# Optimization experiments

Measured on AMD Instinct MI355X. Metric: run time of the kernel, lower is better.

## Reference

```python
import jax, jax.numpy as jnp
import numpy as np
from jax import lax

B, T, I, H, O = 256, 512, 64, 128, 2  # batch, seq_len, input_size, hidden_size, output_size


def gru_layer(x, Wih, Whh, bih, bhh, reverse):
    # x: [B,T,in_dim], Wih: [3H,in_dim], Whh: [3H,H]; PyTorch gate order: r, z, n
    xw = jnp.einsum('bti,gi->btg', x, Wih) + bih  # precompute input projections [B,T,3H]

    def step(h, xw_t):
        gh = h @ Whh.T + bhh  # [B,3H]
        r = jax.nn.sigmoid(xw_t[:, :H] + gh[:, :H])
        z = jax.nn.sigmoid(xw_t[:, H:2 * H] + gh[:, H:2 * H])
        n = jnp.tanh(xw_t[:, 2 * H:] + r * gh[:, 2 * H:])
        h_new = (1.0 - z) * n + z * h
        return h_new, h_new

    h0 = jnp.zeros((x.shape[0], H), x.dtype)
    _, hs = lax.scan(step, h0, jnp.swapaxes(xw, 0, 1), reverse=reverse)
    # lax.scan with reverse=True stacks outputs aligned to original time order,
    # matching PyTorch's bidirectional GRU output layout.
    return jnp.swapaxes(hs, 0, 1)  # [B,T,H]


def gru_forward(x, params, fc_w, fc_b):
    h = x
    for (Wf, Uf, bf, cf, Wb, Ub, bb, cb) in params:
        fwd = gru_layer(h, Wf, Uf, bf, cf, reverse=False)
        bwd = gru_layer(h, Wb, Ub, bb, cb, reverse=True)
        h = jnp.concatenate([fwd, bwd], axis=-1)  # [B,T,2H]
    last = jax.nn.relu(h[:, -1, :])  # relu then take last timestep (equivalent order)
    return last @ fc_w.T + fc_b  # [B,O]


def setup_inputs() -> dict:
    key = jax.random.key(0)
    ks = iter(jax.random.split(key, 24))
    s = 1.0 / np.sqrt(H)  # PyTorch GRU init scale
    u = lambda shape: jax.random.uniform(next(ks), shape, jnp.float32, -s, s)
    inp = {"x": jax.random.normal(next(ks), (B, T, I), jnp.float32)}
    for l, in_dim in enumerate([I, 2 * H]):
        for d in ("f", "b"):
            inp[f"Wih{l}{d}"] = u((3 * H, in_dim))
            inp[f"Whh{l}{d}"] = u((3 * H, H))
            inp[f"bih{l}{d}"] = u((3 * H,))
            inp[f"bhh{l}{d}"] = u((3 * H,))
    inp["fc_w"] = u((O, 2 * H))
    inp["fc_b"] = u((O,))
    return inp


def reference(x, Wih0f, Whh0f, bih0f, bhh0f, Wih0b, Whh0b, bih0b, bhh0b,
              Wih1f, Whh1f, bih1f, bhh1f, Wih1b, Whh1b, bih1b, bhh1b,
              fc_w, fc_b):
    params = [(Wih0f, Whh0f, bih0f, bhh0f, Wih0b, Whh0b, bih0b, bhh0b),
              (Wih1f, Whh1f, bih1f, bhh1f, Wih1b, Whh1b, bih1b, bhh1b)]
    return gru_forward(x, params, fc_w, fc_b)
```

## Files before the change

kernel.cpp:

```cpp
#include <hip/hip_runtime.h>
#include <hip/hip_fp16.h>

#define B_  256
#define T_  512
#define I_  64
#define H_  128
#define G_  384
#define HC  256

#define O_OUT0 0ull
#define O_XW1  67108864ull
#define O_X16  O_XW1
#define O_WP   167772160ull
#define O_H1F  (O_WP + 196608ull)
#define O_WF16 (O_H1F + 131072ull)

typedef _Float16 h8 __attribute__((ext_vector_type(8)));
typedef _Float16 h2 __attribute__((ext_vector_type(2)));
typedef float    f4 __attribute__((ext_vector_type(4)));

#define MFMA16 __builtin_amdgcn_mfma_f32_16x16x32_f16

__device__ __forceinline__ float sigm(float x)   { return __builtin_amdgcn_rcpf(1.f + __expf(-x)); }
__device__ __forceinline__ float tanh_f(float x) { return 1.f - 2.f * __builtin_amdgcn_rcpf(1.f + __expf(2.f * x)); }

__device__ __forceinline__ void bar_lds() {
    asm volatile("s_waitcnt lgkmcnt(0)\n\ts_barrier" ::: "memory");
}

__device__ __forceinline__ h8 load_w8(const float* src) {
    f4 a = *(const f4*)src;
    f4 b = *(const f4*)(src + 4);
    h8 v;
    v[0]=(_Float16)a[0]; v[1]=(_Float16)a[1]; v[2]=(_Float16)a[2]; v[3]=(_Float16)a[3];
    v[4]=(_Float16)b[0]; v[5]=(_Float16)b[1]; v[6]=(_Float16)b[2]; v[7]=(_Float16)b[3];
    return v;
}

__global__ void prep(const float* __restrict__ x, _Float16* __restrict__ x16,
                     const float* __restrict__ Wf, _Float16* __restrict__ wf16,
                     const float* __restrict__ W1b, __half2* __restrict__ wp) {
    const int bid = blockIdx.x;
    const int tid = threadIdx.x;
    if (bid < 4096) {
        int i = bid * 256 + tid;
        const float* s = x + (size_t)i * 8;
        f4 a = *(const f4*)s, b = *(const f4*)(s + 4);
        h8 v;
        v[0]=(_Float16)a[0]; v[1]=(_Float16)a[1]; v[2]=(_Float16)a[2]; v[3]=(_Float16)a[3];
        v[4]=(_Float16)b[0]; v[5]=(_Float16)b[1]; v[6]=(_Float16)b[2]; v[7]=(_Float16)b[3];
        *(h8*)(x16 + (size_t)i * 8) = v;
    } else if (bid < 4144) {
        int i = (bid - 4096) * 256 + tid;
        const float* s = Wf + (size_t)i * 8;
        f4 a = *(const f4*)s, b = *(const f4*)(s + 4);
        h8 v;
        v[0]=(_Float16)a[0]; v[1]=(_Float16)a[1]; v[2]=(_Float16)a[2]; v[3]=(_Float16)a[3];
        v[4]=(_Float16)b[0]; v[5]=(_Float16)b[1]; v[6]=(_Float16)b[2]; v[7]=(_Float16)b[3];
        *(h8*)(wf16 + (size_t)i * 8) = v;
    } else {
        int i = (bid - 4144) * 256 + tid;
        int c = i % G_;
        int k2 = i / G_;
        wp[i] = __halves2half2(__float2half(W1b[c * 256 + 2 * k2]),
                               __float2half(W1b[c * 256 + 2 * k2 + 1]));
    }
}

__launch_bounds__(512, 1)
__global__ void scan_l0(const _Float16* __restrict__ x16,
                        const float* __restrict__ Wih_f, const float* __restrict__ Whh_f,
                        const float* __restrict__ bih_f, const float* __restrict__ bhh_f,
                        const float* __restrict__ Wih_b, const float* __restrict__ Whh_b,
                        const float* __restrict__ bih_b, const float* __restrict__ bhh_b,
                        _Float16* __restrict__ out0) {
    __shared__ __align__(16) _Float16 s_h[2][16 * 128];

    const int tid  = threadIdx.x;
    const int lane = tid & 63;
    const int w    = tid >> 6;
    const int dir  = blockIdx.y;
    const int b0   = blockIdx.x * 4;

    const float* Wih = dir ? Wih_b : Wih_f;
    const float* Whh = dir ? Whh_b : Whh_f;
    const float* bih = dir ? bih_b : bih_f;
    const float* bhh = dir ? bhh_b : bhh_f;

    for (int i = tid; i < 2 * 16 * 128; i += 512) ((_Float16*)s_h)[i] = (_Float16)0.f;

    const int ln15 = lane & 15;
    const int lq   = lane >> 4;
    const int col  = 16 * w + ln15;

    h8 bh[3][4], bx[3][2];
    float seedR = bih[col] + bhh[col];
    float seedZ = bih[H_ + col] + bhh[H_ + col];
    float bihN  = bih[2 * H_ + col];
    float bhhN  = bhh[2 * H_ + col];
#pragma unroll
    for (int g = 0; g < 3; g++) {
        int n = g * H_ + col;
#pragma unroll
        for (int kt = 0; kt < 4; kt++) bh[g][kt] = load_w8(Whh + (size_t)n * H_ + kt * 32 + lq * 8);
#pragma unroll
        for (int kt = 0; kt < 2; kt++) bx[g][kt] = load_w8(Wih + (size_t)n * I_ + kt * 32 + lq * 8);
    }
    const int arow = ln15 & 12;
    int offh[4];
#pragma unroll
    for (int kt = 0; kt < 4; kt++)
        offh[kt] = arow * 128 + (((kt * 4 + lq) ^ arow) & 15) * 8;
    const int row0  = lq * 4;
    const int offw0 = row0 * 128 + ((((col >> 3) ^ row0) & 15)) * 8 + (col & 7);

    const f4 z4 = (f4){0.f, 0.f, 0.f, 0.f};
    const f4 sR4 = (f4){seedR, seedR, seedR, seedR};
    const f4 sZ4 = (f4){seedZ, seedZ, seedZ, seedZ};
    const f4 sXn4 = (f4){bihN, bihN, bihN, bihN};
    const f4 sHn4 = (f4){bhhN, bhhN, bhhN, bhhN};

    const int tbit = (ln15 >> 1) & 1;
    const _Float16* xpb = x16 + ((size_t)(b0 + (ln15 >> 2)) * T_ + (dir ? (T_ - 1 - tbit) : tbit)) * I_ + lq * 8;
    const int xIterStep = dir ? -(2 * I_) : (2 * I_);

    _Float16* op = out0 + ((size_t)(b0 + lq) * T_ + (dir ? (T_ - 1) : 0)) * HC + dir * H_ + col;
    const int ostep = dir ? -HC : HC;

    float hF = 0.f;
    float xrA, xzA, xnA, xrB, xzB, xnB;
    float nxrA, nxzA, nxnA, nxrB, nxzB, nxnB;
    h8 xv0, xv1;
    {
        h8 xc0 = *(const h8*)(xpb);
        h8 xc1 = *(const h8*)(xpb + 32);
        xv0 = *(const h8*)(xpb + xIterStep);
        xv1 = *(const h8*)(xpb + xIterStep + 32);
        f4 aXr = sR4, aXz = sZ4, aXn = sXn4;
        aXr = MFMA16(xc0, bx[0][0], aXr, 0, 0, 0);
        aXz = MFMA16(xc0, bx[1][0], aXz, 0, 0, 0);
        aXn = MFMA16(xc0, bx[2][0], aXn, 0, 0, 0);
        aXr = MFMA16(xc1, bx[0][1], aXr, 0, 0, 0);
        aXz = MFMA16(xc1, bx[1][1], aXz, 0, 0, 0);
        aXn = MFMA16(xc1, bx[2][1], aXn, 0, 0, 0);
        xrA = aXr[0]; xzA = aXz[0]; xnA = aXn[0];
        xrB = aXr[2]; xzB = aXz[2]; xnB = aXn[2];
    }
    const _Float16* xp = xpb + 2 * xIterStep;
    __syncthreads();

#pragma unroll 1
    for (int t = 0; t < T_; t += 2) {
        {
            h8 ah0 = *(const h8*)&s_h[0][offh[0]];
            h8 ah1 = *(const h8*)&s_h[0][offh[1]];
            h8 ah2 = *(const h8*)&s_h[0][offh[2]];
            h8 ah3 = *(const h8*)&s_h[0][offh[3]];
            f4 hRa = z4, hRb = z4, hZa = z4, hZb = z4, hNa = sHn4, hNb = z4;
            hRa = MFMA16(ah0, bh[0][0], hRa, 0, 0, 0);
            hZa = MFMA16(ah0, bh[1][0], hZa, 0, 0, 0);
            hNa = MFMA16(ah0, bh[2][0], hNa, 0, 0, 0);
            hRb = MFMA16(ah2, bh[0][2], hRb, 0, 0, 0);
            hZb = MFMA16(ah2, bh[1][2], hZb, 0, 0, 0);
            hNb = MFMA16(ah2, bh[2][2], hNb, 0, 0, 0);
            hRa = MFMA16(ah1, bh[0][1], hRa, 0, 0, 0);
            hZa = MFMA16(ah1, bh[1][1], hZa, 0, 0, 0);
            hNa = MFMA16(ah1, bh[2][1], hNa, 0, 0, 0);
            hRb = MFMA16(ah3, bh[0][3], hRb, 0, 0, 0);
            hZb = MFMA16(ah3, bh[1][3], hZb, 0, 0, 0);
            hNb = MFMA16(ah3, bh[2][3], hNb, 0, 0, 0);
            float r = sigm(xrA + hRa[0] + hRb[0]);
            float z = sigm(xzA + hZa[0] + hZb[0]);
            float n = tanh_f(xnA + r * (hNa[0] + hNb[0]));
            float h = n + z * (hF - n);
            hF = h;
            s_h[1][offw0] = (_Float16)h;
            *op = (_Float16)h; op += ostep;
            if (t + 2 < T_) {
                f4 aXr = sR4, aXz = sZ4, aXn = sXn4;
                aXr = MFMA16(xv0, bx[0][0], aXr, 0, 0, 0);
                aXz = MFMA16(xv0, bx[1][0], aXz, 0, 0, 0);
                aXn = MFMA16(xv0, bx[2][0], aXn, 0, 0, 0);
                aXr = MFMA16(xv1, bx[0][1], aXr, 0, 0, 0);
                aXz = MFMA16(xv1, bx[1][1], aXz, 0, 0, 0);
                aXn = MFMA16(xv1, bx[2][1], aXn, 0, 0, 0);
                nxrA = aXr[0]; nxzA = aXz[0]; nxnA = aXn[0];
                nxrB = aXr[2]; nxzB = aXz[2]; nxnB = aXn[2];
            }
            bar_lds();
        }
        {
            h8 ah0 = *(const h8*)&s_h[1][offh[0]];
            h8 ah1 = *(const h8*)&s_h[1][offh[1]];
            h8 ah2 = *(const h8*)&s_h[1][offh[2]];
            h8 ah3 = *(const h8*)&s_h[1][offh[3]];
            f4 hRa = z4, hRb = z4, hZa = z4, hZb = z4, hNa = sHn4, hNb = z4;
            hRa = MFMA16(ah0, bh[0][0], hRa, 0, 0, 0);
            hZa = MFMA16(ah0, bh[1][0], hZa, 0, 0, 0);
            hNa = MFMA16(ah0, bh[2][0], hNa, 0, 0, 0);
            hRb = MFMA16(ah2, bh[0][2], hRb, 0, 0, 0);
            hZb = MFMA16(ah2, bh[1][2], hZb, 0, 0, 0);
            hNb = MFMA16(ah2, bh[2][2], hNb, 0, 0, 0);
            hRa = MFMA16(ah1, bh[0][1], hRa, 0, 0, 0);
            hZa = MFMA16(ah1, bh[1][1], hZa, 0, 0, 0);
            hNa = MFMA16(ah1, bh[2][1], hNa, 0, 0, 0);
            hRb = MFMA16(ah3, bh[0][3], hRb, 0, 0, 0);
            hZb = MFMA16(ah3, bh[1][3], hZb, 0, 0, 0);
            hNb = MFMA16(ah3, bh[2][3], hNb, 0, 0, 0);
            float r = sigm(xrB + hRa[0] + hRb[0]);
            float z = sigm(xzB + hZa[0] + hZb[0]);
            float n = tanh_f(xnB + r * (hNa[0] + hNb[0]));
            float h = n + z * (hF - n);
            hF = h;
            s_h[0][offw0] = (_Float16)h;
            *op = (_Float16)h; op += ostep;
            xrA = nxrA; xzA = nxzA; xnA = nxnA;
            xrB = nxrB; xzB = nxzB; xnB = nxnB;
            if (t + 4 < T_) {
                xv0 = *(const h8*)(xp);
                xv1 = *(const h8*)(xp + 32);
                xp += xIterStep;
            }
            bar_lds();
        }
    }
}

__launch_bounds__(256, 1)
__global__ void gemm_xw1(const _Float16* __restrict__ A,
                         const _Float16* __restrict__ Bw,
                         const float* __restrict__ bias,
                         _Float16* __restrict__ C) {
    __shared__ __align__(16) _Float16 sA[2][64 * 64];
    __shared__ __align__(16) _Float16 sB[2][384 * 64];
    const int tid  = threadIdx.x;
    const int lane = tid & 63;
    const int w    = tid >> 6;
    const int wm   = w & 1, wn = w >> 1;
    const int ln15 = lane & 15, lq = lane >> 4;
    const size_t m0 = (size_t)blockIdx.x * 64;

    f4 acc[2][12] = {};

    int aRow[2], aG[2], aOff[2];
#pragma unroll
    for (int k = 0; k < 2; k++) {
        int idx = k * 256 + tid;
        aRow[k] = idx >> 3; aG[k] = idx & 7;
        aOff[k] = aRow[k] * 64 + ((aG[k] ^ (aRow[k] & 7)) & 7) * 8;
    }
    int bRow[12], bG[12], bOff[12];
#pragma unroll
    for (int k = 0; k < 12; k++) {
        int idx = k * 256 + tid;
        bRow[k] = idx >> 3; bG[k] = idx & 7;
        bOff[k] = bRow[k] * 64 + ((bG[k] ^ (bRow[k] & 7)) & 7) * 8;
    }
    int offA[2][2], offB[12][2];
#pragma unroll
    for (int mt = 0; mt < 2; mt++)
#pragma unroll
        for (int kt = 0; kt < 2; kt++) {
            int row = wm * 32 + mt * 16 + ln15;
            offA[mt][kt] = row * 64 + (((kt * 4 + lq) ^ (row & 7)) & 7) * 8;
        }
#pragma unroll
    for (int nt = 0; nt < 12; nt++)
#pragma unroll
        for (int kt = 0; kt < 2; kt++) {
            int row = wn * 192 + nt * 16 + ln15;
            offB[nt][kt] = row * 64 + (((kt * 4 + lq) ^ (row & 7)) & 7) * 8;
        }

    {
        h8 av[2], bv[12];
#pragma unroll
        for (int k = 0; k < 2; k++) av[k] = *(const h8*)(A + (m0 + aRow[k]) * 256 + aG[k] * 8);
#pragma unroll
        for (int k = 0; k < 12; k++) bv[k] = *(const h8*)(Bw + (size_t)bRow[k] * 256 + bG[k] * 8);
#pragma unroll
        for (int k = 0; k < 2; k++) *(h8*)&sA[0][aOff[k]] = av[k];
#pragma unroll
        for (int k = 0; k < 12; k++) *(h8*)&sB[0][bOff[k]] = bv[k];
        bar_lds();
    }

#pragma unroll
    for (int c = 0; c < 4; c++) {
        const int cur = c & 1;
        h8 av[2], bv[12];
        if (c < 3) {
#pragma unroll
            for (int k = 0; k < 2; k++)
                av[k] = *(const h8*)(A + (m0 + aRow[k]) * 256 + (c + 1) * 64 + aG[k] * 8);
#pragma unroll
            for (int k = 0; k < 12; k++)
                bv[k] = *(const h8*)(Bw + (size_t)bRow[k] * 256 + (c + 1) * 64 + bG[k] * 8);
        }
#pragma unroll
        for (int kt = 0; kt < 2; kt++) {
            h8 af0 = *(const h8*)&sA[cur][offA[0][kt]];
            h8 af1 = *(const h8*)&sA[cur][offA[1][kt]];
#pragma unroll
            for (int nt = 0; nt < 12; nt++) {
                h8 bf = *(const h8*)&sB[cur][offB[nt][kt]];
                acc[0][nt] = MFMA16(af0, bf, acc[0][nt], 0, 0, 0);
                acc[1][nt] = MFMA16(af1, bf, acc[1][nt], 0, 0, 0);
            }
        }
        if (c < 3) {
#pragma unroll
            for (int k = 0; k < 2; k++) *(h8*)&sA[cur ^ 1][aOff[k]] = av[k];
#pragma unroll
            for (int k = 0; k < 12; k++) *(h8*)&sB[cur ^ 1][bOff[k]] = bv[k];
            bar_lds();
        }
    }
#pragma unroll
    for (int nt = 0; nt < 12; nt++) {
        int col = wn * 192 + nt * 16 + ln15;
        float bb = bias[col];
        int pcol = (col < 256) ? ((col & 127) * 2 + (col >> 7)) : col;
#pragma unroll
        for (int mt = 0; mt < 2; mt++) {
            size_t row = m0 + wm * 32 + mt * 16 + lq * 4;
#pragma unroll
            for (int reg = 0; reg < 4; reg++)
                C[(row + reg) * G_ + pcol] = (_Float16)(acc[mt][nt][reg] + bb);
        }
    }
}

__launch_bounds__(512, 1)
__global__ void scan_l1(const _Float16* __restrict__ xw1,
                        const float* __restrict__ Whh,
                        const float* __restrict__ bhh,
                        float* __restrict__ h1f) {
    __shared__ __align__(16) _Float16 s_h[2][16 * 128];

    const int tid  = threadIdx.x;
    const int lane = tid & 63;
    const int w    = tid >> 6;
    const int b0   = blockIdx.x * 4;

    for (int i = tid; i < 2 * 16 * 128; i += 512) ((_Float16*)s_h)[i] = (_Float16)0.f;

    const int ln15 = lane & 15;
    const int lq   = lane >> 4;
    const int col  = 16 * w + ln15;

    h8 bh[3][4];
    float bhhF[3];
#pragma unroll
    for (int g = 0; g < 3; g++) {
        int n = g * H_ + col;
        bhhF[g] = bhh[n];
#pragma unroll
        for (int kt = 0; kt < 4; kt++) bh[g][kt] = load_w8(Whh + (size_t)n * H_ + kt * 32 + lq * 8);
    }
    const int arow = ln15 & 12;
    int offh[4];
#pragma unroll
    for (int kt = 0; kt < 4; kt++)
        offh[kt] = arow * 128 + (((kt * 4 + lq) ^ arow) & 15) * 8;
    const int row0  = lq * 4;
    const int offw0 = row0 * 128 + ((((col >> 3) ^ row0) & 15)) * 8 + (col & 7);

    const _Float16* rzbase = xw1 + ((size_t)(b0 + lq) * T_) * G_ + 2 * col;
    const _Float16* nbase  = xw1 + ((size_t)(b0 + lq) * T_) * G_ + 256 + col;

    const f4 z4 = (f4){0.f, 0.f, 0.f, 0.f};
    const f4 sR4 = (f4){bhhF[0], bhhF[0], bhhF[0], bhhF[0]};
    const f4 sZ4 = (f4){bhhF[1], bhhF[1], bhhF[1], bhhF[1]};
    const f4 sN4 = (f4){bhhF[2], bhhF[2], bhhF[2], bhhF[2]};

    __syncthreads();

    float hF = 0.f;
    h2 rzA = *(const h2*)(rzbase);
    h2 rzB = *(const h2*)(rzbase + G_);
    _Float16 nA = *nbase;
    _Float16 nB = *(nbase + G_);
    const _Float16* rzP2 = rzbase + 2 * G_;
    const _Float16* nP2  = nbase  + 2 * G_;
    const _Float16* rzP3 = rzbase + 3 * G_;
    const _Float16* nP3  = nbase  + 3 * G_;

#pragma unroll 1
    for (int s = 0; s < T_; s += 2) {
        {
            h8 ah0 = *(const h8*)&s_h[0][offh[0]];
            h8 ah1 = *(const h8*)&s_h[0][offh[1]];
            h8 ah2 = *(const h8*)&s_h[0][offh[2]];
            h8 ah3 = *(const h8*)&s_h[0][offh[3]];
            float xr = (float)rzA[0], xz = (float)rzA[1], xn = (float)nA;
            if (s + 2 < T_) {
                rzA = *(const h2*)rzP2;
                nA  = *nP2;
                rzP2 += 2 * G_; nP2 += 2 * G_;
            }
            f4 hRa = sR4, hRb = z4, hZa = sZ4, hZb = z4, hNa = sN4, hNb = z4;
            hRa = MFMA16(ah0, bh[0][0], hRa, 0, 0, 0);
            hZa = MFMA16(ah0, bh[1][0], hZa, 0, 0, 0);
            hNa = MFMA16(ah0, bh[2][0], hNa, 0, 0, 0);
            hRb = MFMA16(ah2, bh[0][2], hRb, 0, 0, 0);
            hZb = MFMA16(ah2, bh[1][2], hZb, 0, 0, 0);
            hNb = MFMA16(ah2, bh[2][2], hNb, 0, 0, 0);
            hRa = MFMA16(ah1, bh[0][1], hRa, 0, 0, 0);
            hZa = MFMA16(ah1, bh[1][1], hZa, 0, 0, 0);
            hNa = MFMA16(ah1, bh[2][1], hNa, 0, 0, 0);
            hRb = MFMA16(ah3, bh[0][3], hRb, 0, 0, 0);
            hZb = MFMA16(ah3, bh[1][3], hZb, 0, 0, 0);
            hNb = MFMA16(ah3, bh[2][3], hNb, 0, 0, 0);
            float r = sigm(xr + hRa[0] + hRb[0]);
            float z = sigm(xz + hZa[0] + hZb[0]);
            float n = tanh_f(xn + r * (hNa[0] + hNb[0]));
            float h = n + z * (hF - n);
            hF = h;
            s_h[1][offw0] = (_Float16)h;
            bar_lds();
        }
        {
            h8 ah0 = *(const h8*)&s_h[1][offh[0]];
            h8 ah1 = *(const h8*)&s_h[1][offh[1]];
            h8 ah2 = *(const h8*)&s_h[1][offh[2]];
            h8 ah3 = *(const h8*)&s_h[1][offh[3]];
            float xr = (float)rzB[0], xz = (float)rzB[1], xn = (float)nB;
            if (s + 3 < T_) {
                rzB = *(const h2*)rzP3;
                nB  = *nP3;
                rzP3 += 2 * G_; nP3 += 2 * G_;
            }
            f4 hRa = sR4, hRb = z4, hZa = sZ4, hZb = z4, hNa = sN4, hNb = z4;
            hRa = MFMA16(ah0, bh[0][0], hRa, 0, 0, 0);
            hZa = MFMA16(ah0, bh[1][0], hZa, 0, 0, 0);
            hNa = MFMA16(ah0, bh[2][0], hNa, 0, 0, 0);
            hRb = MFMA16(ah2, bh[0][2], hRb, 0, 0, 0);
            hZb = MFMA16(ah2, bh[1][2], hZb, 0, 0, 0);
            hNb = MFMA16(ah2, bh[2][2], hNb, 0, 0, 0);
            hRa = MFMA16(ah1, bh[0][1], hRa, 0, 0, 0);
            hZa = MFMA16(ah1, bh[1][1], hZa, 0, 0, 0);
            hNa = MFMA16(ah1, bh[2][1], hNa, 0, 0, 0);
            hRb = MFMA16(ah3, bh[0][3], hRb, 0, 0, 0);
            hZb = MFMA16(ah3, bh[1][3], hZb, 0, 0, 0);
            hNb = MFMA16(ah3, bh[2][3], hNb, 0, 0, 0);
            float r = sigm(xr + hRa[0] + hRb[0]);
            float z = sigm(xz + hZa[0] + hZb[0]);
            float n = tanh_f(xn + r * (hNa[0] + hNb[0]));
            float h = n + z * (hF - n);
            hF = h;
            s_h[0][offw0] = (_Float16)h;
            bar_lds();
        }
    }
    h1f[(size_t)(b0 + lq) * H_ + col] = hF;
}

__launch_bounds__(384)
__global__ void final_k(const _Float16* __restrict__ out0,
                        const float* __restrict__ h1f,
                        const __half2* __restrict__ w1b,
                        const float* __restrict__ bih1b, const float* __restrict__ bhh1b,
                        const float* __restrict__ fcw, const float* __restrict__ fcb,
                        float* __restrict__ out) {
    __shared__ __align__(16) float s_x1[HC];
    __shared__ __align__(16) float s_xw[G_];
    __shared__ __align__(16) float s_hc[HC];
    __shared__ float s_red[8];
    const int tid = threadIdx.x;
    const int b = blockIdx.x;
    if (tid < HC)
        s_x1[tid] = (float)out0[((size_t)b * T_ + (T_ - 1)) * HC + tid];
    __syncthreads();
    {
        float acc0 = 0.f, acc1 = 0.f;
        const float2* xv = (const float2*)s_x1;
#pragma unroll 8
        for (int k2 = 0; k2 < 128; k2 += 2) {
            float2 w0 = __half22float2(w1b[k2 * G_ + tid]);
            float2 w1 = __half22float2(w1b[(k2 + 1) * G_ + tid]);
            float2 a0 = xv[k2], a1 = xv[k2 + 1];
            acc0 += a0.x * w0.x + a0.y * w0.y;
            acc1 += a1.x * w1.x + a1.y * w1.y;
        }
        s_xw[tid] = bih1b[tid] + acc0 + acc1;
    }
    __syncthreads();
    if (tid < H_) {
        int j = tid;
        float rg = sigm(s_xw[j] + bhh1b[j]);
        float zg = sigm(s_xw[H_ + j] + bhh1b[H_ + j]);
        float ng = tanh_f(s_xw[2 * H_ + j] + rg * bhh1b[2 * H_ + j]);
        float hb = (1.f - zg) * ng;
        s_hc[H_ + j] = fmaxf(hb, 0.f);
        s_hc[j] = fmaxf(h1f[(size_t)b * H_ + j], 0.f);
    }
    __syncthreads();
    if (tid < HC) {
        float hv = s_hc[tid];
        float p0 = hv * fcw[tid];
        float p1 = hv * fcw[HC + tid];
#pragma unroll
        for (int off = 32; off; off >>= 1) {
            p0 += __shfl_down(p0, off);
            p1 += __shfl_down(p1, off);
        }
        if ((tid & 63) == 0) { s_red[(tid >> 6) * 2] = p0; s_red[(tid >> 6) * 2 + 1] = p1; }
    }
    __syncthreads();
    if (tid == 0) {
        out[b * 2 + 0] = fcb[0] + s_red[0] + s_red[2] + s_red[4] + s_red[6];
        out[b * 2 + 1] = fcb[1] + s_red[1] + s_red[3] + s_red[5] + s_red[7];
    }
}

extern "C" void kernel_launch(void* const* d_in, const int* in_sizes, int n_in,
                              void* d_out, int out_size, void* d_ws, size_t ws_size,
                              hipStream_t stream) {
    (void)in_sizes; (void)n_in; (void)out_size; (void)ws_size;
    const float* x     = (const float*)d_in[0];
    const float* Wih0f = (const float*)d_in[1];
    const float* Whh0f = (const float*)d_in[2];
    const float* bih0f = (const float*)d_in[3];
    const float* bhh0f = (const float*)d_in[4];
    const float* Wih0b = (const float*)d_in[5];
    const float* Whh0b = (const float*)d_in[6];
    const float* bih0b = (const float*)d_in[7];
    const float* bhh0b = (const float*)d_in[8];
    const float* Wih1f = (const float*)d_in[9];
    const float* Whh1f = (const float*)d_in[10];
    const float* bih1f = (const float*)d_in[11];
    const float* bhh1f = (const float*)d_in[12];
    const float* Wih1b = (const float*)d_in[13];
    const float* bih1b = (const float*)d_in[15];
    const float* bhh1b = (const float*)d_in[16];
    const float* fcw   = (const float*)d_in[17];
    const float* fcb   = (const float*)d_in[18];

    char* ws = (char*)d_ws;
    _Float16* out0 = (_Float16*)(ws + O_OUT0);
    _Float16* xw1  = (_Float16*)(ws + O_XW1);
    _Float16* x16  = (_Float16*)(ws + O_X16);
    __half2*  wp   = (__half2*)(ws + O_WP);
    float*    h1f  = (float*)(ws + O_H1F);
    _Float16* wf16 = (_Float16*)(ws + O_WF16);
    float*    out  = (float*)d_out;

    prep<<<4336, 256, 0, stream>>>(x, x16, Wih1f, wf16, Wih1b, wp);

    scan_l0<<<dim3(64, 2), 512, 0, stream>>>(x16, Wih0f, Whh0f, bih0f, bhh0f,
                                             Wih0b, Whh0b, bih0b, bhh0b, out0);

    gemm_xw1<<<2048, 256, 0, stream>>>(out0, wf16, bih1f, xw1);

    scan_l1<<<64, 512, 0, stream>>>(xw1, Whh1f, bhh1f, h1f);

    final_k<<<256, 384, 0, stream>>>(out0, h1f, wp, bih1b, bhh1b, fcw, fcb, out);
}
```

Measured before the change: 562.4 us.

## Fuse x fp16 conversion into layer-0 scan and batch input projection over four steps

Drops the separate prep pass that converted the whole fp32 input x to fp16. The layer-0 scan now reads fp32 x directly and converts it in registers. The input projection MFMA now covers four timesteps per call instead of two, using all four accumulator rows, so the input-projection MFMAs and loads run half as often per step. The cost is that the scan's global loads are twice as wide (fp32), and the hidden-state loop is unrolled four ways through a macro.

```diff
diff --git a/kernel.cpp b/kernel.cpp
--- a/kernel.cpp
+++ b/kernel.cpp
@@ -10,7 +10,6 @@
 
 #define O_OUT0 0ull
 #define O_XW1  67108864ull
-#define O_X16  O_XW1
 #define O_WP   167772160ull
 #define O_H1F  (O_WP + 196608ull)
 #define O_WF16 (O_H1F + 131072ull)
@@ -37,21 +36,12 @@
     return v;
 }
 
-__global__ void prep(const float* __restrict__ x, _Float16* __restrict__ x16,
-                     const float* __restrict__ Wf, _Float16* __restrict__ wf16,
+__global__ void prep(const float* __restrict__ Wf, _Float16* __restrict__ wf16,
                      const float* __restrict__ W1b, __half2* __restrict__ wp) {
     const int bid = blockIdx.x;
     const int tid = threadIdx.x;
-    if (bid < 4096) {
+    if (bid < 48) {
         int i = bid * 256 + tid;
-        const float* s = x + (size_t)i * 8;
-        f4 a = *(const f4*)s, b = *(const f4*)(s + 4);
-        h8 v;
-        v[0]=(_Float16)a[0]; v[1]=(_Float16)a[1]; v[2]=(_Float16)a[2]; v[3]=(_Float16)a[3];
-        v[4]=(_Float16)b[0]; v[5]=(_Float16)b[1]; v[6]=(_Float16)b[2]; v[7]=(_Float16)b[3];
-        *(h8*)(x16 + (size_t)i * 8) = v;
-    } else if (bid < 4144) {
-        int i = (bid - 4096) * 256 + tid;
         const float* s = Wf + (size_t)i * 8;
         f4 a = *(const f4*)s, b = *(const f4*)(s + 4);
         h8 v;
@@ -59,7 +49,7 @@
         v[4]=(_Float16)b[0]; v[5]=(_Float16)b[1]; v[6]=(_Float16)b[2]; v[7]=(_Float16)b[3];
         *(h8*)(wf16 + (size_t)i * 8) = v;
     } else {
-        int i = (bid - 4144) * 256 + tid;
+        int i = (bid - 48) * 256 + tid;
         int c = i % G_;
         int k2 = i / G_;
         wp[i] = __halves2half2(__float2half(W1b[c * 256 + 2 * k2]),
@@ -67,8 +57,37 @@
     }
 }
 
+#define L0_STEP(SB, DB, J, ...) do {                                          \
+    h8 ah0 = *(const h8*)&s_h[SB][offh[0]];                                   \
+    h8 ah1 = *(const h8*)&s_h[SB][offh[1]];                                   \
+    h8 ah2 = *(const h8*)&s_h[SB][offh[2]];                                   \
+    h8 ah3 = *(const h8*)&s_h[SB][offh[3]];                                   \
+    f4 hRa = z4, hRb = z4, hZa = z4, hZb = z4, hNa = sHn4, hNb = z4;          \
+    hRa = MFMA16(ah0, bh[0][0], hRa, 0, 0, 0);                                \
+    hZa = MFMA16(ah0, bh[1][0], hZa, 0, 0, 0);                                \
+    hNa = MFMA16(ah0, bh[2][0], hNa, 0, 0, 0);                                \
+    hRb = MFMA16(ah2, bh[0][2], hRb, 0, 0, 0);                                \
+    hZb = MFMA16(ah2, bh[1][2], hZb, 0, 0, 0);                                \
+    hNb = MFMA16(ah2, bh[2][2], hNb, 0, 0, 0);                                \
+    hRa = MFMA16(ah1, bh[0][1], hRa, 0, 0, 0);                                \
+    hZa = MFMA16(ah1, bh[1][1], hZa, 0, 0, 0);                                \
+    hNa = MFMA16(ah1, bh[2][1], hNa, 0, 0, 0);                                \
+    hRb = MFMA16(ah3, bh[0][3], hRb, 0, 0, 0);                                \
+    hZb = MFMA16(ah3, bh[1][3], hZb, 0, 0, 0);                                \
+    hNb = MFMA16(ah3, bh[2][3], hNb, 0, 0, 0);                                \
+    float r_ = sigm(gR[J] + hRa[0] + hRb[0]);                                 \
+    float z_ = sigm(gZ[J] + hZa[0] + hZb[0]);                                 \
+    float n_ = tanh_f(gN[J] + r_ * (hNa[0] + hNb[0]));                        \
+    float h_ = n_ + z_ * (hF - n_);                                           \
+    hF = h_;                                                                  \
+    s_h[DB][offw0] = (_Float16)h_;                                            \
+    *op = (_Float16)h_; op += ostep;                                          \
+    __VA_ARGS__                                                               \
+    bar_lds();                                                                \
+} while (0)
+
 __launch_bounds__(512, 1)
-__global__ void scan_l0(const _Float16* __restrict__ x16,
+__global__ void scan_l0(const float* __restrict__ xf,
                         const float* __restrict__ Wih_f, const float* __restrict__ Whh_f,
                         const float* __restrict__ bih_f, const float* __restrict__ bhh_f,
                         const float* __restrict__ Wih_b, const float* __restrict__ Whh_b,
@@ -120,109 +139,58 @@
     const f4 sXn4 = (f4){bihN, bihN, bihN, bihN};
     const f4 sHn4 = (f4){bhhN, bhhN, bhhN, bhhN};
 
-    const int tbit = (ln15 >> 1) & 1;
-    const _Float16* xpb = x16 + ((size_t)(b0 + (ln15 >> 2)) * T_ + (dir ? (T_ - 1 - tbit) : tbit)) * I_ + lq * 8;
-    const int xIterStep = dir ? -(2 * I_) : (2 * I_);
+    const int toff = ln15 & 3;
+    const float* xp = xf + ((size_t)(b0 + (ln15 >> 2)) * T_ + (dir ? (T_ - 1 - toff) : toff)) * I_ + lq * 8;
+    const int xstep = dir ? -(4 * I_) : (4 * I_);
 
     _Float16* op = out0 + ((size_t)(b0 + lq) * T_ + (dir ? (T_ - 1) : 0)) * HC + dir * H_ + col;
     const int ostep = dir ? -HC : HC;
 
     float hF = 0.f;
-    float xrA, xzA, xnA, xrB, xzB, xnB;
-    float nxrA, nxzA, nxnA, nxrB, nxzB, nxnB;
-    h8 xv0, xv1;
+    f4 gR, gZ, gN;
+    f4 ngR, ngZ, ngN;
+    h8 xvA0, xvA1;
     {
-        h8 xc0 = *(const h8*)(xpb);
-        h8 xc1 = *(const h8*)(xpb + 32);
-        xv0 = *(const h8*)(xpb + xIterStep);
-        xv1 = *(const h8*)(xpb + xIterStep + 32);
-        f4 aXr = sR4, aXz = sZ4, aXn = sXn4;
-        aXr = MFMA16(xc0, bx[0][0], aXr, 0, 0, 0);
-        aXz = MFMA16(xc0, bx[1][0], aXz, 0, 0, 0);
-        aXn = MFMA16(xc0, bx[2][0], aXn, 0, 0, 0);
-        aXr = MFMA16(xc1, bx[0][1], aXr, 0, 0, 0);
-        aXz = MFMA16(xc1, bx[1][1], aXz, 0, 0, 0);
-        aXn = MFMA16(xc1, bx[2][1], aXn, 0, 0, 0);
-        xrA = aXr[0]; xzA = aXz[0]; xnA = aXn[0];
-        xrB = aXr[2]; xzB = aXz[2]; xnB = aXn[2];
-    }
-    const _Float16* xp = xpb + 2 * xIterStep;
+        h8 xc0 = load_w8(xp);
+        h8 xc1 = load_w8(xp + 32);
+        xp += xstep;
+        xvA0 = load_w8(xp);
+        xvA1 = load_w8(xp + 32);
+        xp += xstep;
+        gR = sR4; gZ = sZ4; gN = sXn4;
+        gR = MFMA16(xc0, bx[0][0], gR, 0, 0, 0);
+        gZ = MFMA16(xc0, bx[1][0], gZ, 0, 0, 0);
+        gN = MFMA16(xc0, bx[2][0], gN, 0, 0, 0);
+        gR = MFMA16(xc1, bx[0][1], gR, 0, 0, 0);
+        gZ = MFMA16(xc1, bx[1][1], gZ, 0, 0, 0);
+        gN = MFMA16(xc1, bx[2][1], gN, 0, 0, 0);
+    }
     __syncthreads();
 
 #pragma unroll 1
-    for (int t = 0; t < T_; t += 2) {
-        {
-            h8 ah0 = *(const h8*)&s_h[0][offh[0]];
-            h8 ah1 = *(const h8*)&s_h[0][offh[1]];
-            h8 ah2 = *(const h8*)&s_h[0][offh[2]];
-            h8 ah3 = *(const h8*)&s_h[0][offh[3]];
-            f4 hRa = z4, hRb = z4, hZa = z4, hZb = z4, hNa = sHn4, hNb = z4;
-            hRa = MFMA16(ah0, bh[0][0], hRa, 0, 0, 0);
-            hZa = MFMA16(ah0, bh[1][0], hZa, 0, 0, 0);
-            hNa = MFMA16(ah0, bh[2][0], hNa, 0, 0, 0);
-            hRb = MFMA16(ah2, bh[0][2], hRb, 0, 0, 0);
-            hZb = MFMA16(ah2, bh[1][2], hZb, 0, 0, 0);
-            hNb = MFMA16(ah2, bh[2][2], hNb, 0, 0, 0);
-            hRa = MFMA16(ah1, bh[0][1], hRa, 0, 0, 0);
-            hZa = MFMA16(ah1, bh[1][1], hZa, 0, 0, 0);
-            hNa = MFMA16(ah1, bh[2][1], hNa, 0, 0, 0);
-            hRb = MFMA16(ah3, bh[0][3], hRb, 0, 0, 0);
-            hZb = MFMA16(ah3, bh[1][3], hZb, 0, 0, 0);
-            hNb = MFMA16(ah3, bh[2][3], hNb, 0, 0, 0);
-            float r = sigm(xrA + hRa[0] + hRb[0]);
-            float z = sigm(xzA + hZa[0] + hZb[0]);
-            float n = tanh_f(xnA + r * (hNa[0] + hNb[0]));
-            float h = n + z * (hF - n);
-            hF = h;
-            s_h[1][offw0] = (_Float16)h;
-            *op = (_Float16)h; op += ostep;
-            if (t + 2 < T_) {
-                f4 aXr = sR4, aXz = sZ4, aXn = sXn4;
-                aXr = MFMA16(xv0, bx[0][0], aXr, 0, 0, 0);
-                aXz = MFMA16(xv0, bx[1][0], aXz, 0, 0, 0);
-                aXn = MFMA16(xv0, bx[2][0], aXn, 0, 0, 0);
-                aXr = MFMA16(xv1, bx[0][1], aXr, 0, 0, 0);
-                aXz = MFMA16(xv1, bx[1][1], aXz, 0, 0, 0);
-                aXn = MFMA16(xv1, bx[2][1], aXn, 0, 0, 0);
-                nxrA = aXr[0]; nxzA = aXz[0]; nxnA = aXn[0];
-                nxrB = aXr[2]; nxzB = aXz[2]; nxnB = aXn[2];
+    for (int t = 0; t < T_; t += 4) {
+        L0_STEP(0, 1, 0,
+            if (t + 4 < T_) {
+                ngR = sR4; ngZ = sZ4; ngN = sXn4;
+                ngR = MFMA16(xvA0, bx[0][0], ngR, 0, 0, 0);
+                ngZ = MFMA16(xvA0, bx[1][0], ngZ, 0, 0, 0);
+                ngN = MFMA16(xvA0, bx[2][0], ngN, 0, 0, 0);
+                ngR = MFMA16(xvA1, bx[0][1], ngR, 0, 0, 0);
+                ngZ = MFMA16(xvA1, bx[1][1], ngZ, 0, 0, 0);
+                ngN = MFMA16(xvA1, bx[2][1], ngN, 0, 0, 0);
             }
-            bar_lds();
-        }
-        {
-            h8 ah0 = *(const h8*)&s_h[1][offh[0]];
-            h8 ah1 = *(const h8*)&s_h[1][offh[1]];
-            h8 ah2 = *(const h8*)&s_h[1][offh[2]];
-            h8 ah3 = *(const h8*)&s_h[1][offh[3]];
-            f4 hRa = z4, hRb = z4, hZa = z4, hZb = z4, hNa = sHn4, hNb = z4;
-            hRa = MFMA16(ah0, bh[0][0], hRa, 0, 0, 0);
-            hZa = MFMA16(ah0, bh[1][0], hZa, 0, 0, 0);
-            hNa = MFMA16(ah0, bh[2][0], hNa, 0, 0, 0);
-            hRb = MFMA16(ah2, bh[0][2], hRb, 0, 0, 0);
-            hZb = MFMA16(ah2, bh[1][2], hZb, 0, 0, 0);
-            hNb = MFMA16(ah2, bh[2][2], hNb, 0, 0, 0);
-            hRa = MFMA16(ah1, bh[0][1], hRa, 0, 0, 0);
-            hZa = MFMA16(ah1, bh[1][1], hZa, 0, 0, 0);
-            hNa = MFMA16(ah1, bh[2][1], hNa, 0, 0, 0);
-            hRb = MFMA16(ah3, bh[0][3], hRb, 0, 0, 0);
-            hZb = MFMA16(ah3, bh[1][3], hZb, 0, 0, 0);
-            hNb = MFMA16(ah3, bh[2][3], hNb, 0, 0, 0);
-            float r = sigm(xrB + hRa[0] + hRb[0]);
-            float z = sigm(xzB + hZa[0] + hZb[0]);
-            float n = tanh_f(xnB + r * (hNa[0] + hNb[0]));
-            float h = n + z * (hF - n);
-            hF = h;
-            s_h[0][offw0] = (_Float16)h;
-            *op = (_Float16)h; op += ostep;
-            xrA = nxrA; xzA = nxzA; xnA = nxnA;
-            xrB = nxrB; xzB = nxzB; xnB = nxnB;
-            if (t + 4 < T_) {
-                xv0 = *(const h8*)(xp);
-                xv1 = *(const h8*)(xp + 32);
-                xp += xIterStep;
+        );
+        L0_STEP(1, 0, 1, );
+        L0_STEP(0, 1, 2,
+            if (t + 8 < T_) {
+                xvA0 = load_w8(xp);
+                xvA1 = load_w8(xp + 32);
+                xp += xstep;
             }
-            bar_lds();
-        }
+        );
+        L0_STEP(1, 0, 3,
+            gR = ngR; gZ = ngZ; gN = ngN;
+        );
     }
 }
 
@@ -540,15 +508,14 @@
     char* ws = (char*)d_ws;
     _Float16* out0 = (_Float16*)(ws + O_OUT0);
     _Float16* xw1  = (_Float16*)(ws + O_XW1);
-    _Float16* x16  = (_Float16*)(ws + O_X16);
     __half2*  wp   = (__half2*)(ws + O_WP);
     float*    h1f  = (float*)(ws + O_H1F);
     _Float16* wf16 = (_Float16*)(ws + O_WF16);
     float*    out  = (float*)d_out;
 
-    prep<<<4336, 256, 0, stream>>>(x, x16, Wih1f, wf16, Wih1b, wp);
-
-    scan_l0<<<dim3(64, 2), 512, 0, stream>>>(x16, Wih0f, Whh0f, bih0f, bhh0f,
+    prep<<<240, 256, 0, stream>>>(Wih1f, wf16, Wih1b, wp);
+
+    scan_l0<<<dim3(64, 2), 512, 0, stream>>>(x, Wih0f, Whh0f, bih0f, bhh0f,
                                              Wih0b, Whh0b, bih0b, bhh0b, out0);
 
     gemm_xw1<<<2048, 256, 0, stream>>>(out0, wf16, bih1f, xw1);
```

New measurement: 681.9 us. +21.2%, slower.
